# Optimization experiments

Measured on AMD Instinct MI355X. Metric: run time of the kernel, lower is better.

The kernel has to match this reference:

```python
import jax, jax.numpy as jnp
import numpy as np

B, N, H, S, NH = 4, 32768, 256, 64, 8
HD = H // NH  # head dim = 32
EPS = 1e-5


def _ln(x, g, b):
    mu = jnp.mean(x, axis=-1, keepdims=True)
    var = jnp.mean(jnp.square(x - mu), axis=-1, keepdims=True)
    return (x - mu) * jax.lax.rsqrt(var + EPS) * g + b


def setup_inputs() -> dict:
    key = jax.random.key(0)
    ks = jax.random.split(key, 16)
    sc = lambda *shape: 0.02
    d = {
        "x": jax.random.normal(ks[0], (B, N, H), jnp.float32),
        "sq_w": jax.random.normal(ks[1], (S, H), jnp.float32) * 0.02,
        "sq_b": jnp.zeros((S,), jnp.float32),
        "eid_state": jnp.zeros((1, S, H), jnp.float32),
        "eid_gw": jax.random.normal(ks[2], (H, H), jnp.float32) * 0.02,
        "eid_gb": jnp.zeros((H,), jnp.float32),
        "in_w": jax.random.normal(ks[3], (3 * H, H), jnp.float32) * 0.02,
        "in_b": jnp.zeros((3 * H,), jnp.float32),
        "out_w": jax.random.normal(ks[4], (H, H), jnp.float32) * 0.02,
        "out_b": jnp.zeros((H,), jnp.float32),
        "n1_g": jnp.ones((H,), jnp.float32),
        "n1_b": jnp.zeros((H,), jnp.float32),
        "n2_g": jnp.ones((H,), jnp.float32),
        "n2_b": jnp.zeros((H,), jnp.float32),
        "f1_w": jax.random.normal(ks[5], (4 * H, H), jnp.float32) * 0.02,
        "f1_b": jnp.zeros((4 * H,), jnp.float32),
        "f2_w": jax.random.normal(ks[6], (H, 4 * H), jnp.float32) * 0.02,
        "f2_b": jnp.zeros((H,), jnp.float32),
    }
    return d


def reference(x, sq_w, sq_b, eid_state, eid_gw, eid_gb, in_w, in_b,
              out_w, out_b, n1_g, n1_b, n2_g, n2_b, f1_w, f1_b, f2_w, f2_b):
    # soft slot assignment: W [B,N,S]
    W = jax.nn.softmax(jnp.einsum('bnh,sh->bns', x, sq_w) + sq_b, axis=-1)
    # pool to slice tokens [B,S,H]
    st = jnp.einsum('bns,bnh->bsh', W, x)
    # eidetic gating
    gate = jax.nn.sigmoid(jnp.einsum('bsh,gh->bsg', st, eid_gw) + eid_gb)
    st = st + gate * eid_state
    # multi-head self-attention over slices
    qkv = jnp.einsum('bsh,oh->bso', st, in_w) + in_b  # [B,S,3H]
    q, k, v = jnp.split(qkv, 3, axis=-1)
    q = q.reshape(B, S, NH, HD)
    k = k.reshape(B, S, NH, HD)
    v = v.reshape(B, S, NH, HD)
    scores = jnp.einsum('bqnd,bknd->bnqk', q, k) / np.float32(np.sqrt(HD))
    attn = jax.nn.softmax(scores, axis=-1)
    ao = jnp.einsum('bnqk,bknd->bqnd', attn, v).reshape(B, S, H)
    ao = jnp.einsum('bsh,oh->bso', ao, out_w) + out_b
    st = _ln(st + ao, n1_g, n1_b)
    # FFN (exact GELU, matching torch nn.GELU default)
    h = jax.nn.gelu(jnp.einsum('bsh,fh->bsf', st, f1_w) + f1_b, approximate=False)
    ffn = jnp.einsum('bsf,hf->bsh', h, f2_w) + f2_b
    st = _ln(st + ffn, n2_g, n2_b)
    # decode back to mesh points
    out = jnp.einsum('bns,bsh->bnh', W, st)
    return out + x
```

## Files before the change

### kernel.cpp

```cpp
#include <hip/hip_runtime.h>
#include <cstdint>
#include <cstddef>

#define BB  4
#define NN  32768
#define HH  256
#define SS  64
#define NHH 8
#define HDD 32

typedef __attribute__((ext_vector_type(8))) short s16x8;
typedef __attribute__((ext_vector_type(4))) float f32x4;

__device__ __forceinline__ float dot4(const float4 a, const float4 b) {
    return a.x * b.x + a.y * b.y + a.z * b.z + a.w * b.w;
}

__device__ __forceinline__ unsigned bf16r1(float f) {
    unsigned u = __float_as_uint(f);
    u += 0x7FFFu + ((u >> 16) & 1u);
    return u >> 16;
}
__device__ __forceinline__ unsigned bf16pk(float lo, float hi) {
    return bf16r1(lo) | (bf16r1(hi) << 16);
}

__global__ __launch_bounds__(256, 4)
void k1a_scores(const float* __restrict__ x, const float* __restrict__ sq_w,
                const float* __restrict__ sq_b, unsigned short* __restrict__ Wb)
{
    __shared__ unsigned sw[64 * 132];
    const int t = threadIdx.x;
    {
        const int r = t >> 2, q = t & 3;
        const float4* src = (const float4*)(sq_w + r * HH + q * 64);
        unsigned* dst = sw + r * 132 + q * 32;
#pragma unroll
        for (int i = 0; i < 16; ++i) {
            float4 v = src[i];
            dst[2 * i]     = bf16pk(v.x, v.y);
            dst[2 * i + 1] = bf16pk(v.z, v.w);
        }
    }
    const int lane = t & 63, w = t >> 6;
    const int n16 = lane & 15, quad = lane >> 4;
    const int b = blockIdx.x >> 8;
    const int tok0 = (blockIdx.x & 255) * 128 + w * 32;
    const float* xb = x + ((size_t)b * NN + tok0) * HH;

    f32x4 acc[2][4];
#pragma unroll
    for (int mt = 0; mt < 2; ++mt)
#pragma unroll
        for (int nt = 0; nt < 4; ++nt) acc[mt][nt] = (f32x4)(0.f);

    __syncthreads();

    for (int kc = 0; kc < 8; ++kc) {
        union { unsigned u[4]; s16x8 s; } af[2];
#pragma unroll
        for (int mt = 0; mt < 2; ++mt) {
            const float* ap = xb + (size_t)(mt * 16 + n16) * HH + kc * 32 + quad * 8;
            float4 v0 = ((const float4*)ap)[0];
            float4 v1 = ((const float4*)ap)[1];
            af[mt].u[0] = bf16pk(v0.x, v0.y);
            af[mt].u[1] = bf16pk(v0.z, v0.w);
            af[mt].u[2] = bf16pk(v1.x, v1.y);
            af[mt].u[3] = bf16pk(v1.z, v1.w);
        }
#pragma unroll
        for (int nt = 0; nt < 4; ++nt) {
            union { uint4 u; s16x8 s; } bf;
            bf.u = *((const uint4*)(sw + (nt * 16 + n16) * 132 + kc * 16 + quad * 4));
#pragma unroll
            for (int mt = 0; mt < 2; ++mt)
                acc[mt][nt] = __builtin_amdgcn_mfma_f32_16x16x32_bf16(af[mt].s, bf.s, acc[mt][nt], 0, 0, 0);
        }
    }

    const float sb0 = sq_b[n16], sb1 = sq_b[16 + n16], sb2 = sq_b[32 + n16], sb3 = sq_b[48 + n16];
#pragma unroll
    for (int mt = 0; mt < 2; ++mt) {
#pragma unroll
        for (int r = 0; r < 4; ++r) {
            float v0 = acc[mt][0][r] + sb0;
            float v1 = acc[mt][1][r] + sb1;
            float v2 = acc[mt][2][r] + sb2;
            float v3 = acc[mt][3][r] + sb3;
            float m = fmaxf(fmaxf(v0, v1), fmaxf(v2, v3));
#pragma unroll
            for (int msk = 1; msk < 16; msk <<= 1) m = fmaxf(m, __shfl_xor(m, msk));
            float e0 = __expf(v0 - m), e1 = __expf(v1 - m), e2 = __expf(v2 - m), e3 = __expf(v3 - m);
            float s = e0 + e1 + e2 + e3;
#pragma unroll
            for (int msk = 1; msk < 16; msk <<= 1) s += __shfl_xor(s, msk);
            const float inv = 1.f / s;
            unsigned short* wp = Wb + ((size_t)b * NN + tok0 + mt * 16 + quad * 4 + r) * SS;
            wp[n16]      = (unsigned short)bf16r1(e0 * inv);
            wp[16 + n16] = (unsigned short)bf16r1(e1 * inv);
            wp[32 + n16] = (unsigned short)bf16r1(e2 * inv);
            wp[48 + n16] = (unsigned short)bf16r1(e3 * inv);
        }
    }
}

__global__ __launch_bounds__(256, 2)
void k1b_pool(const float* __restrict__ x, const unsigned short* __restrict__ Wb,
              float* __restrict__ partial)
{
    __shared__ unsigned xt[256 * 20];
    __shared__ unsigned wt[64 * 20];
    const int t = threadIdx.x;
    const int lane = t & 63, w = t >> 6;
    const int n16 = lane & 15, quad = lane >> 4;
    const int b = blockIdx.x >> 7;
    const int c = blockIdx.x & 127;
    const float* xb = x + (size_t)b * NN * HH;
    const unsigned short* wbb = Wb + (size_t)b * NN * SS;

    const int sp = t & 15;
    const int shb = t >> 4;

    f32x4 acc[16];
#pragma unroll
    for (int nt = 0; nt < 16; ++nt) acc[nt] = (f32x4)(0.f);

    for (int kc = 0; kc < 8; ++kc) {
        const int tk0 = c * 256 + kc * 32;
        __syncthreads();
        {
            const float* r0 = xb + (size_t)(tk0 + 2 * sp) * HH + shb * 16;
            const float* r1 = r0 + HH;
#pragma unroll
            for (int i = 0; i < 4; ++i) {
                float4 a = ((const float4*)r0)[i];
                float4 bq = ((const float4*)r1)[i];
                unsigned* d = xt + (shb * 16 + i * 4) * 20 + sp;
                d[0]  = bf16pk(a.x, bq.x);
                d[20] = bf16pk(a.y, bq.y);
                d[40] = bf16pk(a.z, bq.z);
                d[60] = bf16pk(a.w, bq.w);
            }
        }
        {
            const unsigned short* w0 = wbb + (size_t)(tk0 + 2 * sp) * SS + shb * 4;
            const unsigned short* w1 = w0 + SS;
            ushort4 a = *((const ushort4*)w0);
            ushort4 bq = *((const ushort4*)w1);
            unsigned* d = wt + (shb * 4) * 20 + sp;
            d[0]  = (unsigned)a.x | ((unsigned)bq.x << 16);
            d[20] = (unsigned)a.y | ((unsigned)bq.y << 16);
            d[40] = (unsigned)a.z | ((unsigned)bq.z << 16);
            d[60] = (unsigned)a.w | ((unsigned)bq.w << 16);
        }
        __syncthreads();
        union { uint4 u; s16x8 s; } av;
        av.u = *((const uint4*)(wt + (w * 16 + n16) * 20 + quad * 4));
#pragma unroll
        for (int nt = 0; nt < 16; ++nt) {
            union { uint4 u; s16x8 s; } bv;
            bv.u = *((const uint4*)(xt + (nt * 16 + n16) * 20 + quad * 4));
            acc[nt] = __builtin_amdgcn_mfma_f32_16x16x32_bf16(av.s, bv.s, acc[nt], 0, 0, 0);
        }
    }
    float* pb = partial + ((size_t)(b * 128 + c) * SS) * HH;
#pragma unroll
    for (int nt = 0; nt < 16; ++nt) {
#pragma unroll
        for (int r = 0; r < 4; ++r)
            pb[(size_t)(w * 16 + quad * 4 + r) * HH + nt * 16 + n16] = acc[nt][r];
    }
}

__global__ __launch_bounds__(256)
void k1c_reduce(const float* __restrict__ partial, float* __restrict__ st0)
{
    const int gid = blockIdx.x * 256 + threadIdx.x;
    const int b = gid >> 14, rem = gid & 16383;
    const float* p = partial + (size_t)b * 128 * 16384 + rem;
    float s = 0.f;
#pragma unroll 8
    for (int c = 0; c < 128; ++c) s += p[(size_t)c * 16384];
    st0[gid] = s;
}

__global__ __launch_bounds__(256)
void mk1a_gate(const float* __restrict__ st0, const float* __restrict__ eid_state,
               const float* __restrict__ gw, const float* __restrict__ gb,
               float* __restrict__ st2)
{
    __shared__ __align__(16) float srow[4][HH];
    const int s = blockIdx.x, t = threadIdx.x;
#pragma unroll
    for (int b = 0; b < 4; ++b) srow[b][t] = st0[(b * SS + s) * HH + t];
    __syncthreads();
    float acc[4] = {0.f, 0.f, 0.f, 0.f};
    const float4* wr = (const float4*)(gw + (size_t)t * HH);
    for (int k = 0; k < HH; k += 4) {
        float4 wv = wr[k >> 2];
#pragma unroll
        for (int b = 0; b < 4; ++b) acc[b] += dot4(*(const float4*)(&srow[b][k]), wv);
    }
    const float bias = gb[t];
    const float es = eid_state[s * HH + t];
#pragma unroll
    for (int b = 0; b < 4; ++b) {
        float gate = 1.f / (1.f + __expf(-(acc[b] + bias)));
        st2[(b * SS + s) * HH + t] = srow[b][t] + gate * es;
    }
}

__global__ __launch_bounds__(256)
void mk1b_qkv(const float* __restrict__ st2, const float* __restrict__ in_w,
              const float* __restrict__ in_b, float* __restrict__ qkv)
{
    __shared__ __align__(16) float srow[4][HH];
    const int s = blockIdx.x / 3, third = blockIdx.x % 3;
    const int t = threadIdx.x;
#pragma unroll
    for (int b = 0; b < 4; ++b) srow[b][t] = st2[(b * SS + s) * HH + t];
    __syncthreads();
    const int o = third * 256 + t;
    float acc[4] = {0.f, 0.f, 0.f, 0.f};
    const float4* wr = (const float4*)(in_w + (size_t)o * HH);
    for (int k = 0; k < HH; k += 4) {
        float4 wv = wr[k >> 2];
#pragma unroll
        for (int b = 0; b < 4; ++b) acc[b] += dot4(*(const float4*)(&srow[b][k]), wv);
    }
    const float bias = in_b[o];
#pragma unroll
    for (int b = 0; b < 4; ++b) qkv[(b * SS + s) * 768 + o] = acc[b] + bias;
}

__global__ __launch_bounds__(64)
void mk2_attn(const float* __restrict__ qkv, float* __restrict__ ao)
{
    __shared__ __align__(16) float Ks[SS][36], Vs[SS][36];
    const int b = blockIdx.x >> 3, nh = blockIdx.x & 7;
    const int qi = threadIdx.x;
    const float* base = qkv + (size_t)(b * SS + qi) * 768 + nh * HDD;
    float q[HDD];
#pragma unroll
    for (int d = 0; d < HDD; d += 4) {
        float4 v = *(const float4*)(base + d);
        q[d] = v.x; q[d + 1] = v.y; q[d + 2] = v.z; q[d + 3] = v.w;
        *(float4*)(&Ks[qi][d]) = *(const float4*)(base + 256 + d);
        *(float4*)(&Vs[qi][d]) = *(const float4*)(base + 512 + d);
    }
    __syncthreads();
    float sc[SS];
#pragma unroll
    for (int ki = 0; ki < SS; ++ki) {
        float a = 0.f;
#pragma unroll
        for (int d = 0; d < HDD; ++d) a += q[d] * Ks[ki][d];
        sc[ki] = a * 0.17677669529663687f;
    }
    float m = sc[0];
#pragma unroll
    for (int ki = 1; ki < SS; ++ki) m = fmaxf(m, sc[ki]);
    float ssum = 0.f;
#pragma unroll
    for (int ki = 0; ki < SS; ++ki) { sc[ki] = __expf(sc[ki] - m); ssum += sc[ki]; }
    const float inv = 1.f / ssum;
    float o[HDD];
#pragma unroll
    for (int d = 0; d < HDD; ++d) o[d] = 0.f;
#pragma unroll
    for (int ki = 0; ki < SS; ++ki) {
        const float p = sc[ki] * inv;
#pragma unroll
        for (int d = 0; d < HDD; ++d) o[d] += p * Vs[ki][d];
    }
    float* aob = ao + (size_t)(b * SS + qi) * HH + nh * HDD;
#pragma unroll
    for (int d = 0; d < HDD; d += 4)
        *(float4*)(aob + d) = make_float4(o[d], o[d + 1], o[d + 2], o[d + 3]);
}

__device__ __forceinline__ void block_reduce_2(float& v1, float& v2, float* lds8)
{
#pragma unroll
    for (int m = 32; m; m >>= 1) { v1 += __shfl_xor(v1, m); v2 += __shfl_xor(v2, m); }
    const int w = threadIdx.x >> 6;
    __syncthreads();
    if ((threadIdx.x & 63) == 0) { lds8[w] = v1; lds8[4 + w] = v2; }
    __syncthreads();
    v1 = lds8[0] + lds8[1] + lds8[2] + lds8[3];
    v2 = lds8[4] + lds8[5] + lds8[6] + lds8[7];
}

__global__ __launch_bounds__(256)
void mk3_outln(const float* __restrict__ ao, const float* __restrict__ out_w,
               const float* __restrict__ out_b, const float* __restrict__ st2,
               const float* __restrict__ n1g, const float* __restrict__ n1b,
               float* __restrict__ st3)
{
    __shared__ __align__(16) float arow[4][HH];
    __shared__ float red[8];
    const int s = blockIdx.x, t = threadIdx.x;
#pragma unroll
    for (int b = 0; b < 4; ++b) arow[b][t] = ao[(b * SS + s) * HH + t];
    __syncthreads();
    float acc[4] = {0.f, 0.f, 0.f, 0.f};
    const float4* wr = (const float4*)(out_w + (size_t)t * HH);
    for (int k = 0; k < HH; k += 4) {
        float4 wv = wr[k >> 2];
#pragma unroll
        for (int b = 0; b < 4; ++b) acc[b] += dot4(*(const float4*)(&arow[b][k]), wv);
    }
    const float ob = out_b[t], g = n1g[t], bt = n1b[t];
#pragma unroll
    for (int b = 0; b < 4; ++b) {
        const float y = st2[(b * SS + s) * HH + t] + acc[b] + ob;
        float s1 = y, s2 = y * y;
        block_reduce_2(s1, s2, red);
        const float mu = s1 * (1.f / HH);
        const float var = s2 * (1.f / HH) - mu * mu;
        const float r = rsqrtf(var + 1e-5f);
        st3[(b * SS + s) * HH + t] = (y - mu) * r * g + bt;
    }
}

__global__ __launch_bounds__(256)
void mk4_ffn1(const float* __restrict__ st3, const float* __restrict__ f1w,
              const float* __restrict__ f1b, float* __restrict__ h1)
{
    __shared__ __align__(16) float srow[4][HH];
    const int s = blockIdx.x >> 2, quarter = blockIdx.x & 3;
    const int t = threadIdx.x;
#pragma unroll
    for (int b = 0; b < 4; ++b) srow[b][t] = st3[(b * SS + s) * HH + t];
    __syncthreads();
    const int o = quarter * 256 + t;
    float acc[4] = {0.f, 0.f, 0.f, 0.f};
    const float4* wr = (const float4*)(f1w + (size_t)o * HH);
    for (int k = 0; k < HH; k += 4) {
        float4 wv = wr[k >> 2];
#pragma unroll
        for (int b = 0; b < 4; ++b) acc[b] += dot4(*(const float4*)(&srow[b][k]), wv);
    }
    const float bias = f1b[o];
#pragma unroll
    for (int b = 0; b < 4; ++b) {
        const float u = acc[b] + bias;
        h1[(b * SS + s) * 1024 + o] = 0.5f * u * (1.f + erff(u * 0.70710678118654752f));
    }
}

__global__ __launch_bounds__(256)
void mk5_ffn2(const float* __restrict__ h1, const float* __restrict__ f2w,
              const float* __restrict__ f2b, const float* __restrict__ st3,
              const float* __restrict__ n2g, const float* __restrict__ n2b,
              float* __restrict__ st4)
{
    __shared__ __align__(16) float hrow[4][1024];
    __shared__ float red[8];
    const int s = blockIdx.x, t = threadIdx.x;
#pragma unroll
    for (int b = 0; b < 4; ++b)
        for (int idx = t; idx < 1024; idx += 256) hrow[b][idx] = h1[(b * SS + s) * 1024 + idx];
    __syncthreads();
    float acc[4] = {0.f, 0.f, 0.f, 0.f};
    const float4* wr = (const float4*)(f2w + (size_t)t * 1024);
    for (int k = 0; k < 1024; k += 4) {
        float4 wv = wr[k >> 2];
#pragma unroll
        for (int b = 0; b < 4; ++b) acc[b] += dot4(*(const float4*)(&hrow[b][k]), wv);
    }
    const float fb = f2b[t], g = n2g[t], bt = n2b[t];
#pragma unroll
    for (int b = 0; b < 4; ++b) {
        const float y = st3[(b * SS + s) * HH + t] + acc[b] + fb;
        float s1 = y, s2 = y * y;
        block_reduce_2(s1, s2, red);
        const float mu = s1 * (1.f / HH);
        const float var = s2 * (1.f / HH) - mu * mu;
        const float r = rsqrtf(var + 1e-5f);
        st4[(b * SS + s) * HH + t] = (y - mu) * r * g + bt;
    }
}

__global__ __launch_bounds__(256, 3)
void k3_decode(const unsigned short* __restrict__ Wb, const float* __restrict__ st4,
               const float* __restrict__ x, float* __restrict__ out)
{
    __shared__ unsigned s4t[256 * 36];
    const int t = threadIdx.x;
    const int lane = t & 63, w = t >> 6;
    const int n16 = lane & 15, quad = lane >> 4;
    const int b = blockIdx.x >> 9;
    const int c = blockIdx.x & 511;
    const int tok0 = c * 64;
    {
        const int sp = t & 31, hb = t >> 5;
        const float* r0 = st4 + (size_t)(b * SS + 2 * sp) * HH + hb * 32;
        const float* r1 = r0 + HH;
#pragma unroll
        for (int i = 0; i < 8; ++i) {
            float4 a = ((const float4*)r0)[i];
            float4 bq = ((const float4*)r1)[i];
            unsigned* d = s4t + (hb * 32 + i * 4) * 36 + sp;
            d[0]   = bf16pk(a.x, bq.x);
            d[36]  = bf16pk(a.y, bq.y);
            d[72]  = bf16pk(a.z, bq.z);
            d[108] = bf16pk(a.w, bq.w);
        }
    }
    f32x4 acc[16];
#pragma unroll
    for (int nt = 0; nt < 16; ++nt) acc[nt] = (f32x4)(0.f);
    __syncthreads();

    const unsigned short* wrow = Wb + ((size_t)b * NN + tok0 + w * 16 + n16) * SS;
#pragma unroll
    for (int ks = 0; ks < 2; ++ks) {
        union { uint4 u; s16x8 s; } av;
        av.u = *((const uint4*)(wrow + ks * 32 + quad * 8));
#pragma unroll
        for (int nt = 0; nt < 16; ++nt) {
            union { uint4 u; s16x8 s; } bv;
            bv.u = *((const uint4*)(s4t + (nt * 16 + n16) * 36 + ks * 16 + quad * 4));
            acc[nt] = __builtin_amdgcn_mfma_f32_16x16x32_bf16(av.s, bv.s, acc[nt], 0, 0, 0);
        }
    }
    const size_t rb = ((size_t)b * NN + tok0 + w * 16 + quad * 4) * HH;
#pragma unroll
    for (int r = 0; r < 4; ++r) {
#pragma unroll
        for (int nt = 0; nt < 16; ++nt) {
            const size_t o = rb + (size_t)r * HH + nt * 16 + n16;
            out[o] = acc[nt][r] + x[o];
        }
    }
}

extern "C" void kernel_launch(void* const* d_in, const int* in_sizes, int n_in,
                              void* d_out, int out_size, void* d_ws, size_t ws_size,
                              hipStream_t stream)
{
    const float* x         = (const float*)d_in[0];
    const float* sq_w      = (const float*)d_in[1];
    const float* sq_b      = (const float*)d_in[2];
    const float* eid_state = (const float*)d_in[3];
    const float* eid_gw    = (const float*)d_in[4];
    const float* eid_gb    = (const float*)d_in[5];
    const float* in_w      = (const float*)d_in[6];
    const float* in_b      = (const float*)d_in[7];
    const float* out_w     = (const float*)d_in[8];
    const float* out_b     = (const float*)d_in[9];
    const float* n1_g      = (const float*)d_in[10];
    const float* n1_b      = (const float*)d_in[11];
    const float* n2_g      = (const float*)d_in[12];
    const float* n2_b      = (const float*)d_in[13];
    const float* f1_w      = (const float*)d_in[14];
    const float* f1_b      = (const float*)d_in[15];
    const float* f2_w      = (const float*)d_in[16];
    const float* f2_b      = (const float*)d_in[17];

    float* ws = (float*)d_ws;
    unsigned short* Wb = (unsigned short*)ws;
    float* partial = ws + 4194304;
    float* st0     = partial + 8388608;
    float* st2     = st0 + 65536;
    float* qkv     = st2 + 65536;
    float* ao      = qkv + 196608;
    float* st3     = ao + 65536;
    float* h1      = st3 + 65536;
    float* st4     = h1 + 262144;
    float* out     = (float*)d_out;

    hipLaunchKernelGGL(k1a_scores, dim3(BB * 256), dim3(256), 0, stream,
                       x, sq_w, sq_b, Wb);
    hipLaunchKernelGGL(k1b_pool, dim3(BB * 128), dim3(256), 0, stream,
                       x, Wb, partial);
    hipLaunchKernelGGL(k1c_reduce, dim3(256), dim3(256), 0, stream, partial, st0);
    hipLaunchKernelGGL(mk1a_gate, dim3(SS), dim3(256), 0, stream,
                       st0, eid_state, eid_gw, eid_gb, st2);
    hipLaunchKernelGGL(mk1b_qkv, dim3(SS * 3), dim3(256), 0, stream,
                       st2, in_w, in_b, qkv);
    hipLaunchKernelGGL(mk2_attn, dim3(BB * NHH), dim3(64), 0, stream, qkv, ao);
    hipLaunchKernelGGL(mk3_outln, dim3(SS), dim3(256), 0, stream,
                       ao, out_w, out_b, st2, n1_g, n1_b, st3);
    hipLaunchKernelGGL(mk4_ffn1, dim3(SS * 4), dim3(256), 0, stream,
                       st3, f1_w, f1_b, h1);
    hipLaunchKernelGGL(mk5_ffn2, dim3(SS), dim3(256), 0, stream,
                       h1, f2_w, f2_b, st3, n2_g, n2_b, st4);
    hipLaunchKernelGGL(k3_decode, dim3(BB * 512), dim3(256), 0, stream,
                       Wb, st4, x, out);
}
```

Measured before the change: 493.1 us.

## Fuse score/softmax with pooling, merge small slice kernels, coalesce decode stores

Merges the score+softmax kernel with the pooling kernel so each block reuses its softmax weights from LDS instead of re-reading them from global memory. The partial-sum reduction, gating and QKV projection are folded into one kernel, and the out-proj/LN/FFN/LN chain into another, which removes several launches and intermediate buffers. The decode epilogue now stages results through LDS so output stores and residual loads are float4-coalesced. The cost is less parallelism in the merged slice kernels (64 blocks doing serial work) and higher register/LDS pressure in the fused first kernel.

Result: slower. 508.1 us (+3.0%).

```diff
diff --git a/kernel.cpp b/kernel.cpp
--- a/kernel.cpp
+++ b/kernel.cpp
@@ -25,16 +25,25 @@
     return bf16r1(lo) | (bf16r1(hi) << 16);
 }
 
-__global__ __launch_bounds__(256, 4)
-void k1a_scores(const float* __restrict__ x, const float* __restrict__ sq_w,
-                const float* __restrict__ sq_b, unsigned short* __restrict__ Wb)
-{
-    __shared__ unsigned sw[64 * 132];
+__global__ __launch_bounds__(256, 2)
+void k1_fused(const float* __restrict__ x, const float* __restrict__ sq_w,
+              const float* __restrict__ sq_b, unsigned short* __restrict__ Wb,
+              float* __restrict__ partial)
+{
+    __shared__ unsigned wt[64 * 132];
+    __shared__ unsigned xt[256 * 20];
     const int t = threadIdx.x;
+    const int lane = t & 63, w = t >> 6;
+    const int n16 = lane & 15, quad = lane >> 4;
+    const int b = blockIdx.x >> 7;
+    const int c = blockIdx.x & 127;
+    const int tok0 = c * 256;
+    const float* xb = x + (size_t)b * NN * HH;
+
     {
         const int r = t >> 2, q = t & 3;
         const float4* src = (const float4*)(sq_w + r * HH + q * 64);
-        unsigned* dst = sw + r * 132 + q * 32;
+        unsigned* dst = wt + r * 132 + q * 32;
 #pragma unroll
         for (int i = 0; i < 16; ++i) {
             float4 v = src[i];
@@ -42,25 +51,19 @@
             dst[2 * i + 1] = bf16pk(v.z, v.w);
         }
     }
-    const int lane = t & 63, w = t >> 6;
-    const int n16 = lane & 15, quad = lane >> 4;
-    const int b = blockIdx.x >> 8;
-    const int tok0 = (blockIdx.x & 255) * 128 + w * 32;
-    const float* xb = x + ((size_t)b * NN + tok0) * HH;
-
-    f32x4 acc[2][4];
-#pragma unroll
-    for (int mt = 0; mt < 2; ++mt)
+    __syncthreads();
+
+    f32x4 acc[4][4];
+#pragma unroll
+    for (int mt = 0; mt < 4; ++mt)
 #pragma unroll
         for (int nt = 0; nt < 4; ++nt) acc[mt][nt] = (f32x4)(0.f);
 
-    __syncthreads();
-
     for (int kc = 0; kc < 8; ++kc) {
-        union { unsigned u[4]; s16x8 s; } af[2];
-#pragma unroll
-        for (int mt = 0; mt < 2; ++mt) {
-            const float* ap = xb + (size_t)(mt * 16 + n16) * HH + kc * 32 + quad * 8;
+        union { unsigned u[4]; s16x8 s; } af[4];
+#pragma unroll
+        for (int mt = 0; mt < 4; ++mt) {
+            const float* ap = xb + (size_t)(tok0 + w * 64 + mt * 16 + n16) * HH + kc * 32 + quad * 8;
             float4 v0 = ((const float4*)ap)[0];
             float4 v1 = ((const float4*)ap)[1];
             af[mt].u[0] = bf16pk(v0.x, v0.y);
@@ -71,16 +74,18 @@
 #pragma unroll
         for (int nt = 0; nt < 4; ++nt) {
             union { uint4 u; s16x8 s; } bf;
-            bf.u = *((const uint4*)(sw + (nt * 16 + n16) * 132 + kc * 16 + quad * 4));
-#pragma unroll
-            for (int mt = 0; mt < 2; ++mt)
+            bf.u = *((const uint4*)(wt + (nt * 16 + n16) * 132 + kc * 16 + quad * 4));
+#pragma unroll
+            for (int mt = 0; mt < 4; ++mt)
                 acc[mt][nt] = __builtin_amdgcn_mfma_f32_16x16x32_bf16(af[mt].s, bf.s, acc[mt][nt], 0, 0, 0);
         }
     }
+    __syncthreads();
 
     const float sb0 = sq_b[n16], sb1 = sq_b[16 + n16], sb2 = sq_b[32 + n16], sb3 = sq_b[48 + n16];
 #pragma unroll
-    for (int mt = 0; mt < 2; ++mt) {
+    for (int mt = 0; mt < 4; ++mt) {
+        float p[4][4];
 #pragma unroll
         for (int r = 0; r < 4; ++r) {
             float v0 = acc[mt][0][r] + sb0;
@@ -95,41 +100,39 @@
 #pragma unroll
             for (int msk = 1; msk < 16; msk <<= 1) s += __shfl_xor(s, msk);
             const float inv = 1.f / s;
-            unsigned short* wp = Wb + ((size_t)b * NN + tok0 + mt * 16 + quad * 4 + r) * SS;
-            wp[n16]      = (unsigned short)bf16r1(e0 * inv);
-            wp[16 + n16] = (unsigned short)bf16r1(e1 * inv);
-            wp[32 + n16] = (unsigned short)bf16r1(e2 * inv);
-            wp[48 + n16] = (unsigned short)bf16r1(e3 * inv);
-        }
-    }
-}
-
-__global__ __launch_bounds__(256, 2)
-void k1b_pool(const float* __restrict__ x, const unsigned short* __restrict__ Wb,
-              float* __restrict__ partial)
-{
-    __shared__ unsigned xt[256 * 20];
-    __shared__ unsigned wt[64 * 20];
-    const int t = threadIdx.x;
-    const int lane = t & 63, w = t >> 6;
-    const int n16 = lane & 15, quad = lane >> 4;
-    const int b = blockIdx.x >> 7;
-    const int c = blockIdx.x & 127;
-    const float* xb = x + (size_t)b * NN * HH;
-    const unsigned short* wbb = Wb + (size_t)b * NN * SS;
-
-    const int sp = t & 15;
-    const int shb = t >> 4;
-
-    f32x4 acc[16];
-#pragma unroll
-    for (int nt = 0; nt < 16; ++nt) acc[nt] = (f32x4)(0.f);
-
+            p[r][0] = e0 * inv; p[r][1] = e1 * inv; p[r][2] = e2 * inv; p[r][3] = e3 * inv;
+        }
+        const int tpb = w * 32 + mt * 8 + quad * 2;
+#pragma unroll
+        for (int j = 0; j < 4; ++j) {
+            wt[(16 * j + n16) * 132 + tpb]     = bf16pk(p[0][j], p[1][j]);
+            wt[(16 * j + n16) * 132 + tpb + 1] = bf16pk(p[2][j], p[3][j]);
+        }
+    }
+    __syncthreads();
+
+    {
+        unsigned* wgd = (unsigned*)(Wb + ((size_t)b * NN + tok0) * SS);
+#pragma unroll
+        for (int i = 0; i < 32; ++i) {
+            const int flat = i * 256 + t;
+            const int token = flat >> 5, dw = flat & 31;
+            const int tp = token >> 1, half = (token & 1) * 16;
+            unsigned lo = wt[(2 * dw) * 132 + tp] >> half;
+            unsigned hi = wt[(2 * dw + 1) * 132 + tp] >> half;
+            wgd[flat] = (lo & 0xFFFFu) | ((hi & 0xFFFFu) << 16);
+        }
+    }
+
+    f32x4 pacc[16];
+#pragma unroll
+    for (int nt = 0; nt < 16; ++nt) pacc[nt] = (f32x4)(0.f);
+
+    const int sp = t & 15, shb = t >> 4;
     for (int kc = 0; kc < 8; ++kc) {
-        const int tk0 = c * 256 + kc * 32;
         __syncthreads();
         {
-            const float* r0 = xb + (size_t)(tk0 + 2 * sp) * HH + shb * 16;
+            const float* r0 = xb + (size_t)(tok0 + kc * 32 + 2 * sp) * HH + shb * 16;
             const float* r1 = r0 + HH;
 #pragma unroll
             for (int i = 0; i < 4; ++i) {
@@ -142,95 +145,78 @@
                 d[60] = bf16pk(a.w, bq.w);
             }
         }
-        {
-            const unsigned short* w0 = wbb + (size_t)(tk0 + 2 * sp) * SS + shb * 4;
-            const unsigned short* w1 = w0 + SS;
-            ushort4 a = *((const ushort4*)w0);
-            ushort4 bq = *((const ushort4*)w1);
-            unsigned* d = wt + (shb * 4) * 20 + sp;
-            d[0]  = (unsigned)a.x | ((unsigned)bq.x << 16);
-            d[20] = (unsigned)a.y | ((unsigned)bq.y << 16);
-            d[40] = (unsigned)a.z | ((unsigned)bq.z << 16);
-            d[60] = (unsigned)a.w | ((unsigned)bq.w << 16);
-        }
         __syncthreads();
         union { uint4 u; s16x8 s; } av;
-        av.u = *((const uint4*)(wt + (w * 16 + n16) * 20 + quad * 4));
+        av.u = *((const uint4*)(wt + (w * 16 + n16) * 132 + kc * 16 + quad * 4));
 #pragma unroll
         for (int nt = 0; nt < 16; ++nt) {
             union { uint4 u; s16x8 s; } bv;
             bv.u = *((const uint4*)(xt + (nt * 16 + n16) * 20 + quad * 4));
-            acc[nt] = __builtin_amdgcn_mfma_f32_16x16x32_bf16(av.s, bv.s, acc[nt], 0, 0, 0);
-        }
-    }
-    float* pb = partial + ((size_t)(b * 128 + c) * SS) * HH;
-#pragma unroll
-    for (int nt = 0; nt < 16; ++nt) {
+            pacc[nt] = __builtin_amdgcn_mfma_f32_16x16x32_bf16(av.s, bv.s, pacc[nt], 0, 0, 0);
+        }
+    }
+    float* pb = partial + (size_t)(b * 128 + c) * SS * HH;
+#pragma unroll
+    for (int nt = 0; nt < 16; ++nt)
 #pragma unroll
         for (int r = 0; r < 4; ++r)
-            pb[(size_t)(w * 16 + quad * 4 + r) * HH + nt * 16 + n16] = acc[nt][r];
-    }
+            pb[(size_t)(w * 16 + quad * 4 + r) * HH + nt * 16 + n16] = pacc[nt][r];
 }
 
 __global__ __launch_bounds__(256)
-void k1c_reduce(const float* __restrict__ partial, float* __restrict__ st0)
-{
-    const int gid = blockIdx.x * 256 + threadIdx.x;
-    const int b = gid >> 14, rem = gid & 16383;
-    const float* p = partial + (size_t)b * 128 * 16384 + rem;
-    float s = 0.f;
-#pragma unroll 8
-    for (int c = 0; c < 128; ++c) s += p[(size_t)c * 16384];
-    st0[gid] = s;
-}
-
-__global__ __launch_bounds__(256)
-void mk1a_gate(const float* __restrict__ st0, const float* __restrict__ eid_state,
-               const float* __restrict__ gw, const float* __restrict__ gb,
-               float* __restrict__ st2)
-{
-    __shared__ __align__(16) float srow[4][HH];
+void mk_pre(const float* __restrict__ partial, const float* __restrict__ eid_state,
+            const float* __restrict__ gw, const float* __restrict__ gb,
+            const float* __restrict__ in_w, const float* __restrict__ in_b,
+            float* __restrict__ st2g, float* __restrict__ qkv)
+{
+    __shared__ __align__(16) float s0[4][HH];
+    __shared__ __align__(16) float s2[4][HH];
     const int s = blockIdx.x, t = threadIdx.x;
-#pragma unroll
-    for (int b = 0; b < 4; ++b) srow[b][t] = st0[(b * SS + s) * HH + t];
-    __syncthreads();
+
+    {
+        const int bb = t >> 6, hq = t & 63;
+        const float* p = partial + ((size_t)(bb * 128) * SS + s) * HH + hq * 4;
+        float4 a = make_float4(0.f, 0.f, 0.f, 0.f);
+        for (int c = 0; c < 128; ++c) {
+            float4 v = *(const float4*)(p + (size_t)c * SS * HH);
+            a.x += v.x; a.y += v.y; a.z += v.z; a.w += v.w;
+        }
+        *(float4*)(&s0[bb][hq * 4]) = a;
+    }
+    __syncthreads();
+
     float acc[4] = {0.f, 0.f, 0.f, 0.f};
     const float4* wr = (const float4*)(gw + (size_t)t * HH);
-    for (int k = 0; k < HH; k += 4) {
-        float4 wv = wr[k >> 2];
-#pragma unroll
-        for (int b = 0; b < 4; ++b) acc[b] += dot4(*(const float4*)(&srow[b][k]), wv);
+    for (int k = 0; k < 64; ++k) {
+        float4 wv = wr[k];
+#pragma unroll
+        for (int bb = 0; bb < 4; ++bb) acc[bb] += dot4(*(const float4*)(&s0[bb][k * 4]), wv);
     }
     const float bias = gb[t];
     const float es = eid_state[s * HH + t];
 #pragma unroll
-    for (int b = 0; b < 4; ++b) {
-        float gate = 1.f / (1.f + __expf(-(acc[b] + bias)));
-        st2[(b * SS + s) * HH + t] = srow[b][t] + gate * es;
-    }
-}
-
-__global__ __launch_bounds__(256)
-void mk1b_qkv(const float* __restrict__ st2, const float* __restrict__ in_w,
-              const float* __restrict__ in_b, float* __restrict__ qkv)
-{
-    __shared__ __align__(16) float srow[4][HH];
-    const int s = blockIdx.x / 3, third = blockIdx.x % 3;
-    const int t = threadIdx.x;
-#pragma unroll
-    for (int b = 0; b < 4; ++b) srow[b][t] = st2[(b * SS + s) * HH + t];
-    __syncthreads();
-    const int o = third * 256 + t;
-    float acc[4] = {0.f, 0.f, 0.f, 0.f};
-    const float4* wr = (const float4*)(in_w + (size_t)o * HH);
-    for (int k = 0; k < HH; k += 4) {
-        float4 wv = wr[k >> 2];
-#pragma unroll
-        for (int b = 0; b < 4; ++b) acc[b] += dot4(*(const float4*)(&srow[b][k]), wv);
-    }
-    const float bias = in_b[o];
-#pragma unroll
-    for (int b = 0; b < 4; ++b) qkv[(b * SS + s) * 768 + o] = acc[b] + bias;
+    for (int bb = 0; bb < 4; ++bb) {
+        float gate = 1.f / (1.f + __expf(-(acc[bb] + bias)));
+        float v = s0[bb][t] + gate * es;
+        s2[bb][t] = v;
+        st2g[(bb * SS + s) * HH + t] = v;
+    }
+    __syncthreads();
+
+#pragma unroll
+    for (int third = 0; third < 3; ++third) {
+        const int o = third * 256 + t;
+        float a4[4] = {0.f, 0.f, 0.f, 0.f};
+        const float4* w2 = (const float4*)(in_w + (size_t)o * HH);
+        for (int k = 0; k < 64; ++k) {
+            float4 wv = w2[k];
+#pragma unroll
+            for (int bb = 0; bb < 4; ++bb) a4[bb] += dot4(*(const float4*)(&s2[bb][k * 4]), wv);
+        }
+        const float ib = in_b[o];
+#pragma unroll
+        for (int bb = 0; bb < 4; ++bb) qkv[(bb * SS + s) * 768 + o] = a4[bb] + ib;
+    }
 }
 
 __global__ __launch_bounds__(64)
@@ -292,101 +278,90 @@
 }
 
 __global__ __launch_bounds__(256)
-void mk3_outln(const float* __restrict__ ao, const float* __restrict__ out_w,
-               const float* __restrict__ out_b, const float* __restrict__ st2,
-               const float* __restrict__ n1g, const float* __restrict__ n1b,
-               float* __restrict__ st3)
+void mk_post(const float* __restrict__ ao, const float* __restrict__ out_w,
+             const float* __restrict__ out_b, const float* __restrict__ st2g,
+             const float* __restrict__ n1g, const float* __restrict__ n1b,
+             const float* __restrict__ f1w, const float* __restrict__ f1b,
+             const float* __restrict__ f2w, const float* __restrict__ f2b,
+             const float* __restrict__ n2g, const float* __restrict__ n2b,
+             float* __restrict__ st4)
 {
     __shared__ __align__(16) float arow[4][HH];
+    __shared__ __align__(16) float s3[4][HH];
+    __shared__ __align__(16) float hbuf[4][1024];
     __shared__ float red[8];
     const int s = blockIdx.x, t = threadIdx.x;
 #pragma unroll
-    for (int b = 0; b < 4; ++b) arow[b][t] = ao[(b * SS + s) * HH + t];
-    __syncthreads();
+    for (int bb = 0; bb < 4; ++bb) arow[bb][t] = ao[(bb * SS + s) * HH + t];
+    __syncthreads();
+
     float acc[4] = {0.f, 0.f, 0.f, 0.f};
     const float4* wr = (const float4*)(out_w + (size_t)t * HH);
-    for (int k = 0; k < HH; k += 4) {
-        float4 wv = wr[k >> 2];
-#pragma unroll
-        for (int b = 0; b < 4; ++b) acc[b] += dot4(*(const float4*)(&arow[b][k]), wv);
-    }
-    const float ob = out_b[t], g = n1g[t], bt = n1b[t];
-#pragma unroll
-    for (int b = 0; b < 4; ++b) {
-        const float y = st2[(b * SS + s) * HH + t] + acc[b] + ob;
-        float s1 = y, s2 = y * y;
-        block_reduce_2(s1, s2, red);
+    for (int k = 0; k < 64; ++k) {
+        float4 wv = wr[k];
+#pragma unroll
+        for (int bb = 0; bb < 4; ++bb) acc[bb] += dot4(*(const float4*)(&arow[bb][k * 4]), wv);
+    }
+    const float ob = out_b[t], g1 = n1g[t], b1 = n1b[t];
+#pragma unroll
+    for (int bb = 0; bb < 4; ++bb) {
+        const float y = st2g[(bb * SS + s) * HH + t] + acc[bb] + ob;
+        float s1 = y, sq = y * y;
+        block_reduce_2(s1, sq, red);
         const float mu = s1 * (1.f / HH);
-        const float var = s2 * (1.f / HH) - mu * mu;
+        const float var = sq * (1.f / HH) - mu * mu;
         const float r = rsqrtf(var + 1e-5f);
-        st3[(b * SS + s) * HH + t] = (y - mu) * r * g + bt;
-    }
-}
-
-__global__ __launch_bounds__(256)
-void mk4_ffn1(const float* __restrict__ st3, const float* __restrict__ f1w,
-              const float* __restrict__ f1b, float* __restrict__ h1)
-{
-    __shared__ __align__(16) float srow[4][HH];
-    const int s = blockIdx.x >> 2, quarter = blockIdx.x & 3;
-    const int t = threadIdx.x;
-#pragma unroll
-    for (int b = 0; b < 4; ++b) srow[b][t] = st3[(b * SS + s) * HH + t];
-    __syncthreads();
-    const int o = quarter * 256 + t;
-    float acc[4] = {0.f, 0.f, 0.f, 0.f};
-    const float4* wr = (const float4*)(f1w + (size_t)o * HH);
-    for (int k = 0; k < HH; k += 4) {
-        float4 wv = wr[k >> 2];
-#pragma unroll
-        for (int b = 0; b < 4; ++b) acc[b] += dot4(*(const float4*)(&srow[b][k]), wv);
-    }
-    const float bias = f1b[o];
-#pragma unroll
-    for (int b = 0; b < 4; ++b) {
-        const float u = acc[b] + bias;
-        h1[(b * SS + s) * 1024 + o] = 0.5f * u * (1.f + erff(u * 0.70710678118654752f));
-    }
-}
-
-__global__ __launch_bounds__(256)
-void mk5_ffn2(const float* __restrict__ h1, const float* __restrict__ f2w,
-              const float* __restrict__ f2b, const float* __restrict__ st3,
-              const float* __restrict__ n2g, const float* __restrict__ n2b,
-              float* __restrict__ st4)
-{
-    __shared__ __align__(16) float hrow[4][1024];
-    __shared__ float red[8];
-    const int s = blockIdx.x, t = threadIdx.x;
-#pragma unroll
-    for (int b = 0; b < 4; ++b)
-        for (int idx = t; idx < 1024; idx += 256) hrow[b][idx] = h1[(b * SS + s) * 1024 + idx];
-    __syncthreads();
-    float acc[4] = {0.f, 0.f, 0.f, 0.f};
-    const float4* wr = (const float4*)(f2w + (size_t)t * 1024);
-    for (int k = 0; k < 1024; k += 4) {
-        float4 wv = wr[k >> 2];
-#pragma unroll
-        for (int b = 0; b < 4; ++b) acc[b] += dot4(*(const float4*)(&hrow[b][k]), wv);
-    }
-    const float fb = f2b[t], g = n2g[t], bt = n2b[t];
-#pragma unroll
-    for (int b = 0; b < 4; ++b) {
-        const float y = st3[(b * SS + s) * HH + t] + acc[b] + fb;
-        float s1 = y, s2 = y * y;
-        block_reduce_2(s1, s2, red);
+        s3[bb][t] = (y - mu) * r * g1 + b1;
+    }
+    __syncthreads();
+
+#pragma unroll
+    for (int q = 0; q < 4; ++q) {
+        const int o = q * 256 + t;
+        float a4[4] = {0.f, 0.f, 0.f, 0.f};
+        const float4* w1 = (const float4*)(f1w + (size_t)o * HH);
+        for (int k = 0; k < 64; ++k) {
+            float4 wv = w1[k];
+#pragma unroll
+            for (int bb = 0; bb < 4; ++bb) a4[bb] += dot4(*(const float4*)(&s3[bb][k * 4]), wv);
+        }
+        const float fb = f1b[o];
+#pragma unroll
+        for (int bb = 0; bb < 4; ++bb) {
+            const float u = a4[bb] + fb;
+            hbuf[bb][o] = 0.5f * u * (1.f + erff(u * 0.70710678118654752f));
+        }
+    }
+    __syncthreads();
+
+    float a2[4] = {0.f, 0.f, 0.f, 0.f};
+    const float4* w2 = (const float4*)(f2w + (size_t)t * 1024);
+    for (int k = 0; k < 256; ++k) {
+        float4 wv = w2[k];
+#pragma unroll
+        for (int bb = 0; bb < 4; ++bb) a2[bb] += dot4(*(const float4*)(&hbuf[bb][k * 4]), wv);
+    }
+    const float fb2 = f2b[t], g2 = n2g[t], b2 = n2b[t];
+#pragma unroll
+    for (int bb = 0; bb < 4; ++bb) {
+        const float y = s3[bb][t] + a2[bb] + fb2;
+        float s1 = y, sq = y * y;
+        block_reduce_2(s1, sq, red);
         const float mu = s1 * (1.f / HH);
-        const float var = s2 * (1.f / HH) - mu * mu;
+        const float var = sq * (1.f / HH) - mu * mu;
         const float r = rsqrtf(var + 1e-5f);
-        st4[(b * SS + s) * HH + t] = (y - mu) * r * g + bt;
-    }
-}
-
-__global__ __launch_bounds__(256, 3)
+        st4[(bb * SS + s) * HH + t] = (y - mu) * r * g2 + b2;
+    }
+}
+
+__global__ __launch_bounds__(256, 4)
 void k3_decode(const unsigned short* __restrict__ Wb, const float* __restrict__ st4,
                const float* __restrict__ x, float* __restrict__ out)
 {
-    __shared__ unsigned s4t[256 * 36];
+    __shared__ union {
+        unsigned s4t[256 * 36];
+        float tb[4][4 * 264];
+    } u;
     const int t = threadIdx.x;
     const int lane = t & 63, w = t >> 6;
     const int n16 = lane & 15, quad = lane >> 4;
@@ -401,7 +376,7 @@
         for (int i = 0; i < 8; ++i) {
             float4 a = ((const float4*)r0)[i];
             float4 bq = ((const float4*)r1)[i];
-            unsigned* d = s4t + (hb * 32 + i * 4) * 36 + sp;
+            unsigned* d = u.s4t + (hb * 32 + i * 4) * 36 + sp;
             d[0]   = bf16pk(a.x, bq.x);
             d[36]  = bf16pk(a.y, bq.y);
             d[72]  = bf16pk(a.z, bq.z);
@@ -416,23 +391,34 @@
     const unsigned short* wrow = Wb + ((size_t)b * NN + tok0 + w * 16 + n16) * SS;
 #pragma unroll
     for (int ks = 0; ks < 2; ++ks) {
-        union { uint4 u; s16x8 s; } av;
-        av.u = *((const uint4*)(wrow + ks * 32 + quad * 8));
+        union { uint4 u4; s16x8 s; } av;
+        av.u4 = *((const uint4*)(wrow + ks * 32 + quad * 8));
 #pragma unroll
         for (int nt = 0; nt < 16; ++nt) {
-            union { uint4 u; s16x8 s; } bv;
-            bv.u = *((const uint4*)(s4t + (nt * 16 + n16) * 36 + ks * 16 + quad * 4));
+            union { uint4 u4; s16x8 s; } bv;
+            bv.u4 = *((const uint4*)(u.s4t + (nt * 16 + n16) * 36 + ks * 16 + quad * 4));
             acc[nt] = __builtin_amdgcn_mfma_f32_16x16x32_bf16(av.s, bv.s, acc[nt], 0, 0, 0);
         }
     }
-    const size_t rb = ((size_t)b * NN + tok0 + w * 16 + quad * 4) * HH;
+    __syncthreads();
+
+    float* tb = u.tb[w];
+    const size_t gbase = (size_t)b * NN + tok0 + w * 16;
 #pragma unroll
     for (int r = 0; r < 4; ++r) {
 #pragma unroll
-        for (int nt = 0; nt < 16; ++nt) {
-            const size_t o = rb + (size_t)r * HH + nt * 16 + n16;
-            out[o] = acc[nt][r] + x[o];
-        }
+        for (int nt = 0; nt < 16; ++nt)
+            tb[quad * 264 + nt * 16 + n16] = acc[nt][r];
+        __syncthreads();
+#pragma unroll
+        for (int q = 0; q < 4; ++q) {
+            const size_t go = (gbase + q * 4 + r) * HH + lane * 4;
+            float4 v = *(const float4*)(tb + q * 264 + lane * 4);
+            float4 xv = *(const float4*)(x + go);
+            v.x += xv.x; v.y += xv.y; v.z += xv.z; v.w += xv.w;
+            *(float4*)(out + go) = v;
+        }
+        __syncthreads();
     }
 }
 
@@ -462,31 +448,20 @@
     float* ws = (float*)d_ws;
     unsigned short* Wb = (unsigned short*)ws;
     float* partial = ws + 4194304;
-    float* st0     = partial + 8388608;
-    float* st2     = st0 + 65536;
+    float* st2     = partial + 8388608;
     float* qkv     = st2 + 65536;
     float* ao      = qkv + 196608;
-    float* st3     = ao + 65536;
-    float* h1      = st3 + 65536;
-    float* st4     = h1 + 262144;
+    float* st4     = ao + 65536;
     float* out     = (float*)d_out;
 
-    hipLaunchKernelGGL(k1a_scores, dim3(BB * 256), dim3(256), 0, stream,
-                       x, sq_w, sq_b, Wb);
-    hipLaunchKernelGGL(k1b_pool, dim3(BB * 128), dim3(256), 0, stream,
-                       x, Wb, partial);
-    hipLaunchKernelGGL(k1c_reduce, dim3(256), dim3(256), 0, stream, partial, st0);
-    hipLaunchKernelGGL(mk1a_gate, dim3(SS), dim3(256), 0, stream,
-                       st0, eid_state, eid_gw, eid_gb, st2);
-    hipLaunchKernelGGL(mk1b_qkv, dim3(SS * 3), dim3(256), 0, stream,
-                       st2, in_w, in_b, qkv);
+    hipLaunchKernelGGL(k1_fused, dim3(BB * 128), dim3(256), 0, stream,
+                       x, sq_w, sq_b, Wb, partial);
+    hipLaunchKernelGGL(mk_pre, dim3(SS), dim3(256), 0, stream,
+                       partial, eid_state, eid_gw, eid_gb, in_w, in_b, st2, qkv);
     hipLaunchKernelGGL(mk2_attn, dim3(BB * NHH), dim3(64), 0, stream, qkv, ao);
-    hipLaunchKernelGGL(mk3_outln, dim3(SS), dim3(256), 0, stream,
-                       ao, out_w, out_b, st2, n1_g, n1_b, st3);
-    hipLaunchKernelGGL(mk4_ffn1, dim3(SS * 4), dim3(256), 0, stream,
-                       st3, f1_w, f1_b, h1);
-    hipLaunchKernelGGL(mk5_ffn2, dim3(SS), dim3(256), 0, stream,
-                       h1, f2_w, f2_b, st3, n2_g, n2_b, st4);
+    hipLaunchKernelGGL(mk_post, dim3(SS), dim3(256), 0, stream,
+                       ao, out_w, out_b, st2, n1_g, n1_b, f1_w, f1_b,
+                       f2_w, f2_b, n2_g, n2_b, st4);
     hipLaunchKernelGGL(k3_decode, dim3(BB * 512), dim3(256), 0, stream,
                        Wb, st4, x, out);
 }
```
